# Kernel optimization log

Measured on AMD Instinct MI355X. Metric: run time of the kernel, lower is better.

## Reference

```python
import jax, jax.numpy as jnp
import numpy as np

B, H, I, T_MAX = 8192, 1024, 128, 128

def setup_inputs() -> dict:
    key = jax.random.key(0)
    k1, k2, k3, k4, k5 = jax.random.split(key, 5)
    s = 1.0 / np.sqrt(I + H)
    return {
        "t": jnp.asarray(37.5, dtype=jnp.float32),
        "h": jax.random.normal(k1, (B, H), dtype=jnp.float32),
        "x_coeffs": jax.random.normal(k2, (T_MAX, B, I), dtype=jnp.float32),
        "W_r": jax.random.normal(k3, (H, I + H), dtype=jnp.float32) * s,
        "W_z": jax.random.normal(k4, (H, I + H), dtype=jnp.float32) * s,
        "W_h": jax.random.normal(k5, (H, I + H), dtype=jnp.float32) * s,
    }

def reference(t, h, x_coeffs, W_r, W_z, W_h):
    time_max = x_coeffs.shape[0]
    t_int = jnp.clip(t.astype(jnp.int32), 0, time_max - 1)
    x = x_coeffs[t_int]                                   # [B, I]
    combined = jnp.concatenate([x, h], axis=1)            # [B, I+H]
    r = jax.nn.sigmoid(combined @ W_r.T)                  # [B, H]
    z = jax.nn.sigmoid(combined @ W_z.T)                  # [B, H]
    combined_rh = jnp.concatenate([x, r * h], axis=1)     # [B, I+H]
    h_tilde = jnp.tanh(combined_rh @ W_h.T)               # [B, H]
    dh = (1.0 - z) * (h_tilde - h)
    return dh
```

## Files before the change

kernel.cpp:

```cpp
#include <hip/hip_runtime.h>
#include <hip/hip_bf16.h>
#include <stdint.h>

#define B_ROWS 8192
#define HDIM   1024
#define IDIM   128
#define KDIM   1152
#define TMAX   128

typedef unsigned short u16;
typedef __bf16 bf16x8 __attribute__((ext_vector_type(8)));
typedef float  f32x4  __attribute__((ext_vector_type(4)));

static __device__ __forceinline__ u16 f2bf(float f) {
  union { float f; unsigned u; } v; v.f = f;
  unsigned r = v.u + 0x7FFFu + ((v.u >> 16) & 1u);
  return (u16)(r >> 16);
}
static __device__ __forceinline__ float bf2f(u16 b) {
  union { unsigned u; float f; } v; v.u = ((unsigned)b) << 16; return v.f;
}

template<int N> __device__ __forceinline__ void waitv() {
  if constexpr (N == 8)      asm volatile("s_waitcnt vmcnt(8)" ::: "memory");
  else if constexpr (N == 6) asm volatile("s_waitcnt vmcnt(6)" ::: "memory");
  else if constexpr (N == 2) asm volatile("s_waitcnt vmcnt(2)" ::: "memory");
  else                       asm volatile("s_waitcnt vmcnt(0)" ::: "memory");
}

#define W_CHUNKS  (3*1024*1152/4)
#define H_CHUNKS  (B_ROWS*HDIM/4)
#define X_CHUNKS  (B_ROWS*IDIM/4)
#define W_BLOCKS  (W_CHUNKS/256)
#define H_BLOCKS  (H_CHUNKS/256)
#define X_BLOCKS  (X_CHUNKS/256)
#define CV_BLOCKS (W_BLOCKS + H_BLOCKS + X_BLOCKS)

__global__ __launch_bounds__(256)
void convert_kernel(const float* __restrict__ t,
                    const float* __restrict__ h,
                    const float* __restrict__ xc,
                    const float* __restrict__ Wr,
                    const float* __restrict__ Wz,
                    const float* __restrict__ Wh,
                    u16* __restrict__ WB,
                    u16* __restrict__ A1)
{
  const int b = blockIdx.x;
  const int tid = threadIdx.x;
  if (b < W_BLOCKS) {
    const int g = b * 256 + tid;
    const int e = g * 4;
    const int S = 1024 * KDIM;
    float4 v;
    if (e < S)            v = *reinterpret_cast<const float4*>(Wr + e);
    else if (e < 2 * S)   v = *reinterpret_cast<const float4*>(Wz + (e - S));
    else                  v = *reinterpret_cast<const float4*>(Wh + (e - 2 * S));
    ushort4 o; o.x = f2bf(v.x); o.y = f2bf(v.y); o.z = f2bf(v.z); o.w = f2bf(v.w);
    *reinterpret_cast<ushort4*>(WB + e) = o;
  } else if (b < W_BLOCKS + H_BLOCKS) {
    const int g = (b - W_BLOCKS) * 256 + tid;
    const int e = g * 4;
    const int row = e >> 10, col = e & 1023;
    float4 v = *reinterpret_cast<const float4*>(h + e);
    ushort4 o; o.x = f2bf(v.x); o.y = f2bf(v.y); o.z = f2bf(v.z); o.w = f2bf(v.w);
    *reinterpret_cast<ushort4*>(A1 + (size_t)row * KDIM + IDIM + col) = o;
  } else {
    const int g = (b - W_BLOCKS - H_BLOCKS) * 256 + tid;
    const int e = g * 4;
    int ti = (int)t[0];
    ti = ti < 0 ? 0 : (ti > TMAX - 1 ? TMAX - 1 : ti);
    const int row = e >> 7, col = e & 127;
    float4 v = *reinterpret_cast<const float4*>(xc + (size_t)ti * B_ROWS * IDIM + e);
    ushort4 o; o.x = f2bf(v.x); o.y = f2bf(v.y); o.z = f2bf(v.z); o.w = f2bf(v.w);
    *reinterpret_cast<ushort4*>(A1 + (size_t)row * KDIM + col) = o;
  }
}

template<int MODE, int NTOT>
__global__ __launch_bounds__(256, 2)
void gemm128(const u16* __restrict__ A, const u16* __restrict__ Ax,
             const u16* __restrict__ W,
             const u16* __restrict__ hb, u16* __restrict__ A2w,
             u16* __restrict__ omz, float* __restrict__ out)
{
  constexpr int NBN  = NTOT / 128;
  constexpr int BMPX = (B_ROWS / 128) / 8;
  constexpr int NT   = KDIM / 64;

  __shared__ u16 As[2][2][64 * 64];
  __shared__ u16 Bs[2][2][64 * 64];

  const int tid  = threadIdx.x;
  const int lane = tid & 63;
  const int wave = tid >> 6;
  const int wm = wave >> 1, wn = wave & 1;
  const int xcd = blockIdx.x & 7, jj = blockIdx.x >> 3;
  const int bm = xcd * BMPX + (jj & (BMPX - 1));
  const int bn = jj / BMPX;
  const int rowBase = bm * 128, colBase = bn * 128;
  const int lr = lane & 15, lkq = lane >> 4;

  auto stA = [&](int buf, int half, int kt) {
    const u16* src = (kt * 64 < IDIM) ? Ax : A;
    #pragma unroll
    for (int rr = 0; rr < 2; ++rr) {
      const int q = rr * 256 + tid;
      const int row = q >> 3, cl = q & 7;
      const int cg = cl ^ (row & 7);
      const u16* g = src + (size_t)(rowBase + half * 64 + row) * KDIM + kt * 64 + cg * 8;
      __builtin_amdgcn_global_load_lds(
          (const __attribute__((address_space(1))) void*)g,
          (__attribute__((address_space(3))) void*)(&As[buf][half][q * 8]), 16, 0, 0);
    }
  };
  auto stB = [&](int buf, int half, int kt) {
    #pragma unroll
    for (int rr = 0; rr < 2; ++rr) {
      const int q = rr * 256 + tid;
      const int row = q >> 3, cl = q & 7;
      const int cg = cl ^ (row & 7);
      const u16* g = W + (size_t)(colBase + half * 64 + row) * KDIM + kt * 64 + cg * 8;
      __builtin_amdgcn_global_load_lds(
          (const __attribute__((address_space(1))) void*)g,
          (__attribute__((address_space(3))) void*)(&Bs[buf][half][q * 8]), 16, 0, 0);
    }
  };

  f32x4 acc[2][2][2][2];
  f32x4 zero = {0.f, 0.f, 0.f, 0.f};
  #pragma unroll
  for (int a = 0; a < 2; ++a)
    #pragma unroll
    for (int b = 0; b < 2; ++b)
      #pragma unroll
      for (int c = 0; c < 2; ++c)
        #pragma unroll
        for (int d = 0; d < 2; ++d) acc[a][b][c][d] = zero;

  bf16x8 bv[2][2][2];
  bf16x8 af[2][2];

  auto rdA = [&](int buf, int half) {
    #pragma unroll
    for (int mf = 0; mf < 2; ++mf)
      #pragma unroll
      for (int kk = 0; kk < 2; ++kk) {
        const int r = wm * 32 + mf * 16 + lr;
        const int c = (kk * 4 + lkq) ^ (r & 7);
        af[mf][kk] = *reinterpret_cast<const bf16x8*>(&As[buf][half][r * 64 + c * 8]);
      }
  };
  auto rdB = [&](int buf) {
    #pragma unroll
    for (int nh = 0; nh < 2; ++nh)
      #pragma unroll
      for (int nf = 0; nf < 2; ++nf)
        #pragma unroll
        for (int kk = 0; kk < 2; ++kk) {
          const int r = wn * 32 + nf * 16 + lr;
          const int c = (kk * 4 + lkq) ^ (r & 7);
          bv[nh][nf][kk] = *reinterpret_cast<const bf16x8*>(&Bs[buf][nh][r * 64 + c * 8]);
        }
  };

#define MFMA_QUAD(MH, NH)                                                       \
    _Pragma("unroll") for (int mf = 0; mf < 2; ++mf)                            \
      _Pragma("unroll") for (int nf = 0; nf < 2; ++nf)                          \
        _Pragma("unroll") for (int kk = 0; kk < 2; ++kk)                        \
          acc[MH][NH][mf][nf] = __builtin_amdgcn_mfma_f32_16x16x32_bf16(        \
              af[mf][kk], bv[NH][nf][kk], acc[MH][NH][mf][nf], 0, 0, 0);

#define PHASE_A(BUF, T, DO_STAGE, WV)  do {                                     \
    rdA(BUF, 0); rdB(BUF);                                                      \
    if (DO_STAGE) stA((BUF) ^ 1, 1, (T) + 1);                                   \
    __builtin_amdgcn_s_barrier();                                               \
    asm volatile("s_waitcnt lgkmcnt(0)" ::: "memory");                          \
    __builtin_amdgcn_s_setprio(1);                                              \
    MFMA_QUAD(0, 0); MFMA_QUAD(0, 1);                                           \
    __builtin_amdgcn_s_setprio(0);                                              \
    waitv<WV>();                                                                \
    __builtin_amdgcn_s_barrier();                                               \
  } while (0)

#define PHASE_B(BUF, T, DO_STAGE, WV)  do {                                     \
    rdA(BUF, 1);                                                                \
    if (DO_STAGE) { stA(BUF, 0, (T) + 2); stB(BUF, 0, (T) + 2);                 \
                    stB(BUF, 1, (T) + 2); }                                     \
    __builtin_amdgcn_s_barrier();                                               \
    asm volatile("s_waitcnt lgkmcnt(0)" ::: "memory");                          \
    __builtin_amdgcn_s_setprio(1);                                              \
    MFMA_QUAD(1, 1); MFMA_QUAD(1, 0);                                           \
    __builtin_amdgcn_s_setprio(0);                                              \
    waitv<WV>();                                                                \
    __builtin_amdgcn_s_barrier();                                               \
  } while (0)

  stA(0, 0, 0); stB(0, 0, 0); stB(0, 1, 0); stA(0, 1, 0);
  stA(1, 0, 1); stB(1, 0, 1); stB(1, 1, 1);
  waitv<6>();
  __builtin_amdgcn_s_barrier();

  for (int t = 0; t < NT - 2; ++t) {
    const int buf = t & 1;
    PHASE_A(buf, t, true, 8);
    PHASE_B(buf, t, true, 8);
  }
  PHASE_A(0, 16, true, 8);
  PHASE_B(0, 16, false, 2);
  PHASE_A(1, 17, false, 0);
  PHASE_B(1, 17, false, 0);

#undef PHASE_A
#undef PHASE_B
#undef MFMA_QUAD

  if (MODE == 0) {
    if (colBase < HDIM) {
      #pragma unroll
      for (int mh = 0; mh < 2; ++mh)
        #pragma unroll
        for (int nh = 0; nh < 2; ++nh)
          #pragma unroll
          for (int mf = 0; mf < 2; ++mf)
            #pragma unroll
            for (int nf = 0; nf < 2; ++nf) {
              f32x4 v = acc[mh][nh][mf][nf];
              const int col = colBase + nh * 64 + wn * 32 + nf * 16 + lr;
              #pragma unroll
              for (int rr = 0; rr < 4; ++rr) {
                const int row = rowBase + mh * 64 + wm * 32 + mf * 16 + lkq * 4 + rr;
                const float sg = 1.f / (1.f + __expf(-v[rr]));
                const float hv = bf2f(hb[(size_t)row * KDIM + IDIM + col]);
                A2w[(size_t)row * KDIM + IDIM + col] = f2bf(sg * hv);
              }
            }
    } else {
      #pragma unroll
      for (int mh = 0; mh < 2; ++mh)
        #pragma unroll
        for (int nh = 0; nh < 2; ++nh)
          #pragma unroll
          for (int mf = 0; mf < 2; ++mf)
            #pragma unroll
            for (int nf = 0; nf < 2; ++nf) {
              f32x4 v = acc[mh][nh][mf][nf];
              const int col = colBase - HDIM + nh * 64 + wn * 32 + nf * 16 + lr;
              #pragma unroll
              for (int rr = 0; rr < 4; ++rr) {
                const int row = rowBase + mh * 64 + wm * 32 + mf * 16 + lkq * 4 + rr;
                const float sg = 1.f / (1.f + __expf(-v[rr]));
                omz[(size_t)row * HDIM + col] = f2bf(1.f - sg);
              }
            }
    }
  } else {
    #pragma unroll
    for (int mh = 0; mh < 2; ++mh)
      #pragma unroll
      for (int nh = 0; nh < 2; ++nh)
        #pragma unroll
        for (int mf = 0; mf < 2; ++mf)
          #pragma unroll
          for (int nf = 0; nf < 2; ++nf) {
            f32x4 v = acc[mh][nh][mf][nf];
            const int col = colBase + nh * 64 + wn * 32 + nf * 16 + lr;
            #pragma unroll
            for (int rr = 0; rr < 4; ++rr) {
              const int row = rowBase + mh * 64 + wm * 32 + mf * 16 + lkq * 4 + rr;
              const float e  = __expf(2.f * v[rr]);
              const float ht = 1.f - 2.f / (e + 1.f);
              const float o  = bf2f(omz[(size_t)row * HDIM + col]);
              const float hv = bf2f(hb[(size_t)row * KDIM + IDIM + col]);
              out[(size_t)row * HDIM + col] = o * (ht - hv);
            }
          }
  }
}

extern "C" void kernel_launch(void* const* d_in, const int* in_sizes, int n_in,
                              void* d_out, int out_size, void* d_ws, size_t ws_size,
                              hipStream_t stream) {
  const float* t  = (const float*)d_in[0];
  const float* h  = (const float*)d_in[1];
  const float* xc = (const float*)d_in[2];
  const float* Wr = (const float*)d_in[3];
  const float* Wz = (const float*)d_in[4];
  const float* Wh = (const float*)d_in[5];
  float* out = (float*)d_out;

  u16* WB  = (u16*)d_ws;
  u16* A1  = WB + (size_t)3 * 1024 * KDIM;
  u16* A2  = A1 + (size_t)B_ROWS * KDIM;
  u16* omz = A2 + (size_t)B_ROWS * KDIM;

  convert_kernel<<<CV_BLOCKS, 256, 0, stream>>>(t, h, xc, Wr, Wz, Wh, WB, A1);

  gemm128<0, 2048><<<1024, 256, 0, stream>>>(A1, A1, WB, A1, A2, omz, out);

  gemm128<1, 1024><<<512, 256, 0, stream>>>(A2, A1, WB + (size_t)2048 * KDIM,
                                            A1, nullptr, omz, out);
}
```

Before: 90.33 us.

## Add 256x256-tile eight-wave GEMM for the r/z gate stage

Replaces the first GEMM (r and z gates, N=2048) with a new kernel using 256x256 output tiles, 512 threads (8 waves), and an 8-phase ping-pong schedule over quarter-tiles. Staging interleaves global-to-LDS loads with MFMA phases and uses setprio around the MFMA blocks. The larger tile raises arithmetic intensity and cuts redundant A/W traffic, but uses 128KB of LDS for one block per CU and leaves only 256 blocks. The second GEMM is split out as its own non-templated kernel and keeps the old schedule.

```diff
diff --git a/kernel.cpp b/kernel.cpp
--- a/kernel.cpp
+++ b/kernel.cpp
@@ -24,6 +24,7 @@
 template<int N> __device__ __forceinline__ void waitv() {
   if constexpr (N == 8)      asm volatile("s_waitcnt vmcnt(8)" ::: "memory");
   else if constexpr (N == 6) asm volatile("s_waitcnt vmcnt(6)" ::: "memory");
+  else if constexpr (N == 4) asm volatile("s_waitcnt vmcnt(4)" ::: "memory");
   else if constexpr (N == 2) asm volatile("s_waitcnt vmcnt(2)" ::: "memory");
   else                       asm volatile("s_waitcnt vmcnt(0)" ::: "memory");
 }
@@ -77,14 +78,177 @@
   }
 }
 
-template<int MODE, int NTOT>
+__global__ __launch_bounds__(512)
+void gemm1_8p(const u16* __restrict__ A, const u16* __restrict__ W,
+              const u16* __restrict__ hb, u16* __restrict__ A2w,
+              u16* __restrict__ omz)
+{
+  constexpr int BMPX  = 32 / 8;
+  constexpr int NT    = KDIM / 64;
+  constexpr int NITER = NT / 2;
+
+  __shared__ u16 As[2][2][128 * 64];
+  __shared__ u16 Bs[2][2][128 * 64];
+
+  const int tid  = threadIdx.x;
+  const int lane = tid & 63;
+  const int wave = tid >> 6;
+  const int wm = wave >> 2, wn = wave & 3;
+  const int xcd = blockIdx.x & 7, jj = blockIdx.x >> 3;
+  const int bm = xcd * BMPX + (jj & (BMPX - 1));
+  const int bn = jj >> 2;
+  const int rowBase = bm * 256, colBase = bn * 256;
+  const int lr = lane & 15, lkq = lane >> 4;
+
+  auto stA = [&](int buf, int half, int kt) {
+    #pragma unroll
+    for (int rr = 0; rr < 2; ++rr) {
+      const int q = rr * 512 + tid;
+      const int row = q >> 3, cl = q & 7;
+      const int cg = cl ^ (row & 7);
+      const u16* g = A + (size_t)(rowBase + half * 128 + row) * KDIM + kt * 64 + cg * 8;
+      __builtin_amdgcn_global_load_lds(
+          (const __attribute__((address_space(1))) void*)g,
+          (__attribute__((address_space(3))) void*)(&As[buf][half][q * 8]), 16, 0, 0);
+    }
+  };
+  auto stB = [&](int buf, int half, int kt) {
+    #pragma unroll
+    for (int rr = 0; rr < 2; ++rr) {
+      const int q = rr * 512 + tid;
+      const int row = q >> 3, cl = q & 7;
+      const int cg = cl ^ (row & 7);
+      const u16* g = W + (size_t)(colBase + half * 128 + row) * KDIM + kt * 64 + cg * 8;
+      __builtin_amdgcn_global_load_lds(
+          (const __attribute__((address_space(1))) void*)g,
+          (__attribute__((address_space(3))) void*)(&Bs[buf][half][q * 8]), 16, 0, 0);
+    }
+  };
+
+  f32x4 acc[2][2][4][2];
+  f32x4 zero = {0.f, 0.f, 0.f, 0.f};
+  #pragma unroll
+  for (int a = 0; a < 2; ++a)
+    #pragma unroll
+    for (int b = 0; b < 2; ++b)
+      #pragma unroll
+      for (int c = 0; c < 4; ++c)
+        #pragma unroll
+        for (int d = 0; d < 2; ++d) acc[a][b][c][d] = zero;
+
+  bf16x8 af[4][2];
+  bf16x8 bv[2][2][2];
+
+  auto rdA = [&](int buf, int half) {
+    #pragma unroll
+    for (int mf = 0; mf < 4; ++mf)
+      #pragma unroll
+      for (int kk = 0; kk < 2; ++kk) {
+        const int r = wm * 64 + mf * 16 + lr;
+        const int c = (kk * 4 + lkq) ^ (r & 7);
+        af[mf][kk] = *reinterpret_cast<const bf16x8*>(&As[buf][half][r * 64 + c * 8]);
+      }
+  };
+  auto rdB = [&](int buf, int half) {
+    #pragma unroll
+    for (int nf = 0; nf < 2; ++nf)
+      #pragma unroll
+      for (int kk = 0; kk < 2; ++kk) {
+        const int r = wn * 32 + nf * 16 + lr;
+        const int c = (kk * 4 + lkq) ^ (r & 7);
+        bv[half][nf][kk] = *reinterpret_cast<const bf16x8*>(&Bs[buf][half][r * 64 + c * 8]);
+      }
+  };
+
+#define MFMA16(MH, NH)                                                          \
+    _Pragma("unroll") for (int mf = 0; mf < 4; ++mf)                            \
+      _Pragma("unroll") for (int nf = 0; nf < 2; ++nf)                          \
+        _Pragma("unroll") for (int kk = 0; kk < 2; ++kk)                        \
+          acc[MH][NH][mf][nf] = __builtin_amdgcn_mfma_f32_16x16x32_bf16(        \
+              af[mf][kk], bv[NH][nf][kk], acc[MH][NH][mf][nf], 0, 0, 0);
+
+#define PH(BUF, MH, NH, RDA, RDB, STG, WT)  do {                                \
+    if (RDA) rdA(BUF, MH);                                                      \
+    if (RDB) rdB(BUF, NH);                                                      \
+    STG                                                                         \
+    __builtin_amdgcn_s_barrier();                                               \
+    asm volatile("s_waitcnt lgkmcnt(0)" ::: "memory");                          \
+    __builtin_amdgcn_s_setprio(1);                                              \
+    MFMA16(MH, NH)                                                              \
+    __builtin_amdgcn_s_setprio(0);                                              \
+    WT                                                                          \
+    __builtin_amdgcn_s_barrier();                                               \
+  } while (0)
+
+  stA(0, 0, 0); stB(0, 0, 0); stA(0, 1, 0); stB(0, 1, 0);
+  stA(1, 0, 1); stB(1, 1, 1);
+  waitv<4>();
+  __builtin_amdgcn_s_barrier();
+
+  for (int i = 0; i < NITER; ++i) {
+    const int T = 2 * i;
+    const bool more = (i < NITER - 1);
+    PH(0, 0, 0, true,  true,  { stA(1, 1, T + 1); stB(1, 0, T + 1); }, {});
+    PH(0, 0, 1, false, true,  {}, {});
+    PH(0, 1, 1, true,  false, { if (more) stA(0, 0, T + 2); }, {});
+    PH(0, 1, 0, false, false, { if (more) stB(0, 1, T + 2); },
+                              { if (more) waitv<4>(); else waitv<0>(); });
+    PH(1, 0, 0, true,  true,  { if (more) { stA(0, 1, T + 2); stB(0, 0, T + 2); } }, {});
+    PH(1, 0, 1, false, true,  {}, {});
+    PH(1, 1, 1, true,  false, { if (more) stA(1, 0, T + 3); }, {});
+    PH(1, 1, 0, false, false, { if (more) stB(1, 1, T + 3); },
+                              { if (more) waitv<4>(); else waitv<0>(); });
+  }
+#undef PH
+#undef MFMA16
+
+  if (colBase < HDIM) {
+    #pragma unroll
+    for (int mh = 0; mh < 2; ++mh)
+      #pragma unroll
+      for (int nh = 0; nh < 2; ++nh)
+        #pragma unroll
+        for (int mf = 0; mf < 4; ++mf)
+          #pragma unroll
+          for (int nf = 0; nf < 2; ++nf) {
+            f32x4 v = acc[mh][nh][mf][nf];
+            const int col = colBase + nh * 128 + wn * 32 + nf * 16 + lr;
+            #pragma unroll
+            for (int rr = 0; rr < 4; ++rr) {
+              const int row = rowBase + mh * 128 + wm * 64 + mf * 16 + lkq * 4 + rr;
+              const float sg = 1.f / (1.f + __expf(-v[rr]));
+              const float hv = bf2f(hb[(size_t)row * KDIM + IDIM + col]);
+              A2w[(size_t)row * KDIM + IDIM + col] = f2bf(sg * hv);
+            }
+          }
+  } else {
+    #pragma unroll
+    for (int mh = 0; mh < 2; ++mh)
+      #pragma unroll
+      for (int nh = 0; nh < 2; ++nh)
+        #pragma unroll
+        for (int mf = 0; mf < 4; ++mf)
+          #pragma unroll
+          for (int nf = 0; nf < 2; ++nf) {
+            f32x4 v = acc[mh][nh][mf][nf];
+            const int col = colBase - HDIM + nh * 128 + wn * 32 + nf * 16 + lr;
+            #pragma unroll
+            for (int rr = 0; rr < 4; ++rr) {
+              const int row = rowBase + mh * 128 + wm * 64 + mf * 16 + lkq * 4 + rr;
+              const float sg = 1.f / (1.f + __expf(-v[rr]));
+              omz[(size_t)row * HDIM + col] = f2bf(1.f - sg);
+            }
+          }
+  }
+}
+
 __global__ __launch_bounds__(256, 2)
-void gemm128(const u16* __restrict__ A, const u16* __restrict__ Ax,
-             const u16* __restrict__ W,
-             const u16* __restrict__ hb, u16* __restrict__ A2w,
-             u16* __restrict__ omz, float* __restrict__ out)
+void gemm2_128(const u16* __restrict__ A, const u16* __restrict__ Ax,
+               const u16* __restrict__ W,
+               const u16* __restrict__ hb, const u16* __restrict__ omz,
+               float* __restrict__ out)
 {
-  constexpr int NBN  = NTOT / 128;
+  constexpr int NBN  = 1024 / 128;
   constexpr int BMPX = (B_ROWS / 128) / 8;
   constexpr int NT   = KDIM / 64;
 
@@ -215,67 +379,26 @@
 #undef PHASE_B
 #undef MFMA_QUAD
 
-  if (MODE == 0) {
-    if (colBase < HDIM) {
-      #pragma unroll
-      for (int mh = 0; mh < 2; ++mh)
-        #pragma unroll
-        for (int nh = 0; nh < 2; ++nh)
+  #pragma unroll
+  for (int mh = 0; mh < 2; ++mh)
+    #pragma unroll
+    for (int nh = 0; nh < 2; ++nh)
+      #pragma unroll
+      for (int mf = 0; mf < 2; ++mf)
+        #pragma unroll
+        for (int nf = 0; nf < 2; ++nf) {
+          f32x4 v = acc[mh][nh][mf][nf];
+          const int col = colBase + nh * 64 + wn * 32 + nf * 16 + lr;
           #pragma unroll
-          for (int mf = 0; mf < 2; ++mf)
-            #pragma unroll
-            for (int nf = 0; nf < 2; ++nf) {
-              f32x4 v = acc[mh][nh][mf][nf];
-              const int col = colBase + nh * 64 + wn * 32 + nf * 16 + lr;
-              #pragma unroll
-              for (int rr = 0; rr < 4; ++rr) {
-                const int row = rowBase + mh * 64 + wm * 32 + mf * 16 + lkq * 4 + rr;
-                const float sg = 1.f / (1.f + __expf(-v[rr]));
-                const float hv = bf2f(hb[(size_t)row * KDIM + IDIM + col]);
-                A2w[(size_t)row * KDIM + IDIM + col] = f2bf(sg * hv);
-              }
-            }
-    } else {
-      #pragma unroll
-      for (int mh = 0; mh < 2; ++mh)
-        #pragma unroll
-        for (int nh = 0; nh < 2; ++nh)
-          #pragma unroll
-          for (int mf = 0; mf < 2; ++mf)
-            #pragma unroll
-            for (int nf = 0; nf < 2; ++nf) {
-              f32x4 v = acc[mh][nh][mf][nf];
-              const int col = colBase - HDIM + nh * 64 + wn * 32 + nf * 16 + lr;
-              #pragma unroll
-              for (int rr = 0; rr < 4; ++rr) {
-                const int row = rowBase + mh * 64 + wm * 32 + mf * 16 + lkq * 4 + rr;
-                const float sg = 1.f / (1.f + __expf(-v[rr]));
-                omz[(size_t)row * HDIM + col] = f2bf(1.f - sg);
-              }
-            }
-    }
-  } else {
-    #pragma unroll
-    for (int mh = 0; mh < 2; ++mh)
-      #pragma unroll
-      for (int nh = 0; nh < 2; ++nh)
-        #pragma unroll
-        for (int mf = 0; mf < 2; ++mf)
-          #pragma unroll
-          for (int nf = 0; nf < 2; ++nf) {
-            f32x4 v = acc[mh][nh][mf][nf];
-            const int col = colBase + nh * 64 + wn * 32 + nf * 16 + lr;
-            #pragma unroll
-            for (int rr = 0; rr < 4; ++rr) {
-              const int row = rowBase + mh * 64 + wm * 32 + mf * 16 + lkq * 4 + rr;
-              const float e  = __expf(2.f * v[rr]);
-              const float ht = 1.f - 2.f / (e + 1.f);
-              const float o  = bf2f(omz[(size_t)row * HDIM + col]);
-              const float hv = bf2f(hb[(size_t)row * KDIM + IDIM + col]);
-              out[(size_t)row * HDIM + col] = o * (ht - hv);
-            }
+          for (int rr = 0; rr < 4; ++rr) {
+            const int row = rowBase + mh * 64 + wm * 32 + mf * 16 + lkq * 4 + rr;
+            const float e  = __expf(2.f * v[rr]);
+            const float ht = 1.f - 2.f / (e + 1.f);
+            const float o  = bf2f(omz[(size_t)row * HDIM + col]);
+            const float hv = bf2f(hb[(size_t)row * KDIM + IDIM + col]);
+            out[(size_t)row * HDIM + col] = o * (ht - hv);
           }
-  }
+        }
 }
 
 extern "C" void kernel_launch(void* const* d_in, const int* in_sizes, int n_in,
@@ -296,8 +419,8 @@
 
   convert_kernel<<<CV_BLOCKS, 256, 0, stream>>>(t, h, xc, Wr, Wz, Wh, WB, A1);
 
-  gemm128<0, 2048><<<1024, 256, 0, stream>>>(A1, A1, WB, A1, A2, omz, out);
-
-  gemm128<1, 1024><<<512, 256, 0, stream>>>(A2, A1, WB + (size_t)2048 * KDIM,
-                                            A1, nullptr, omz, out);
-}
+  gemm1_8p<<<256, 512, 0, stream>>>(A1, WB, A1, A2, omz);
+
+  gemm2_128<<<512, 256, 0, stream>>>(A2, A1, WB + (size_t)2048 * KDIM,
+                                     A1, omz, out);
+}
```

Result: no change. 90.66 us (+0.4%).
